# Performance work log

Measured on AMD Instinct MI355X. Metric: run time of the kernel, lower is better.

The kernel has to match this reference:

```python
import jax, jax.numpy as jnp
import numpy as np

B, T, C = 2, 2048, 1024
H, DK, DV = 16, 64, 64


def setup_inputs() -> dict:
    key = jax.random.key(0)
    ks = jax.random.split(key, 12)
    p = lambda k, shape: (jax.random.normal(k, shape, dtype=jnp.float32) * 0.02)
    Q = jax.random.normal(ks[0], (B, T, C), dtype=jnp.float32)
    K = jax.random.normal(ks[1], (B, T, C), dtype=jnp.float32)
    V = jax.random.normal(ks[2], (B, T, C), dtype=jnp.float32)
    Wq, bq = p(ks[3], (C, H * DK)), p(ks[4], (H * DK,))
    Wk, bk = p(ks[5], (C, H * DK)), p(ks[6], (H * DK,))
    Wv, bv = p(ks[7], (C, H * DV)), p(ks[8], (H * DV,))
    Wo, bo = p(ks[9], (H * DV, C)), p(ks[10], (C,))
    # additive causal mask, broadcastable to (B, H, T, T)
    causal = jnp.tril(jnp.ones((T, T), dtype=bool))
    mask = jnp.where(causal, 0.0, -1e9).astype(jnp.float32)[None, None]
    return {"Q": Q, "K": K, "V": V, "Wq": Wq, "bq": bq, "Wk": Wk, "bk": bk,
            "Wv": Wv, "bv": bv, "Wo": Wo, "bo": bo, "mask": mask}


def reference(Q, K, V, Wq, bq, Wk, bk, Wv, bv, Wo, bo, mask):
    def split(x, d):  # (B,T,H*d) -> (B,H,T,d)
        return x.reshape(B, T, H, d).transpose(0, 2, 1, 3)

    q = split(Q @ Wq + bq, DK)
    k = split(K @ Wk + bk, DK)
    v = split(V @ Wv + bv, DV)
    # NOTE: faithful to source — mask added BEFORE scaling by 1/sqrt(dk)
    scores = (jnp.einsum('bhqd,bhkd->bhqk', q, k) + mask) / float(np.sqrt(DK))
    attn = jax.nn.softmax(scores, axis=-1)
    out = jnp.einsum('bhqk,bhkd->bhqd', attn, v)  # (B,H,T,DV)
    out = out.transpose(0, 2, 1, 3).reshape(B, T, H * DV)
    return out @ Wo + bo
```

## Files before the change

### kernel.cpp

```cpp
#include <hip/hip_runtime.h>
#include <cstdint>
#include <cstddef>

#define TB 2
#define TT 2048
#define TC 1024
#define TH 16
#define TD 64
#define MROWS (TB*TT)

typedef __attribute__((ext_vector_type(8))) short bf16x8;
typedef __attribute__((ext_vector_type(4))) float f32x4;

#define QSCL2 0.18033688011112042f
#define MASKL2 (-1.8033688e8f)

__device__ __forceinline__ unsigned short f2bf(float f) {
  union { float f; unsigned int u; } x; x.f = f;
  unsigned int r = x.u + 0x7fffu + ((x.u >> 16) & 1u);
  return (unsigned short)(r >> 16);
}

__device__ __forceinline__ void gload16(const void* g, void* l) {
  __builtin_amdgcn_global_load_lds((const __attribute__((address_space(1))) void*)g,
                                   (__attribute__((address_space(3))) void*)l, 16, 0, 0);
}

#define WAITVM(N) do { asm volatile("s_waitcnt vmcnt(" #N ")" ::: "memory"); \
                       __builtin_amdgcn_sched_barrier(0); } while (0)

__device__ __forceinline__ float exp2h(float x) {
  float r;
  asm("v_exp_f32 %0, %1" : "=v"(r) : "v"(x));
  return r;
}

__global__ __launch_bounds__(256) void wtrans4_kernel(
    const float* __restrict__ W0, const float* __restrict__ W1,
    const float* __restrict__ W2, const float* __restrict__ W3,
    unsigned short* __restrict__ T0, unsigned short* __restrict__ T1,
    unsigned short* __restrict__ T2, unsigned short* __restrict__ T3) {
  const int z = blockIdx.z;
  const float* W = z == 0 ? W0 : (z == 1 ? W1 : (z == 2 ? W2 : W3));
  unsigned short* WT = z == 0 ? T0 : (z == 1 ? T1 : (z == 2 ? T2 : T3));
  __shared__ float ts[32][33];
  int tx = threadIdx.x & 31, ty = threadIdx.x >> 5;
  int n0 = blockIdx.x * 32, k0 = blockIdx.y * 32;
#pragma unroll
  for (int r = 0; r < 32; r += 8)
    ts[ty + r][tx] = W[(size_t)(k0 + ty + r) * TC + n0 + tx];
  __syncthreads();
#pragma unroll
  for (int r = 0; r < 32; r += 8)
    WT[(size_t)(n0 + ty + r) * TC + k0 + tx] = f2bf(ts[tx][ty + r]);
}

__global__ __launch_bounds__(256) void cast3_kernel(
    const float* __restrict__ A, const float* __restrict__ B, const float* __restrict__ C,
    unsigned short* __restrict__ oa, unsigned short* __restrict__ ob,
    unsigned short* __restrict__ oc) {
  const int z = blockIdx.y;
  const float* in = z == 0 ? A : (z == 1 ? B : C);
  unsigned short* out = z == 0 ? oa : (z == 1 ? ob : oc);
  int i = (blockIdx.x * 256 + threadIdx.x) * 8;
  float4 f0 = *(const float4*)(in + i);
  float4 f1 = *(const float4*)(in + i + 4);
  union { unsigned short u[8]; int4 v; } pk;
  pk.u[0] = f2bf(f0.x); pk.u[1] = f2bf(f0.y); pk.u[2] = f2bf(f0.z); pk.u[3] = f2bf(f0.w);
  pk.u[4] = f2bf(f1.x); pk.u[5] = f2bf(f1.y); pk.u[6] = f2bf(f1.z); pk.u[7] = f2bf(f1.w);
  *(int4*)(out + i) = pk.v;
}

__device__ __forceinline__ void gemm_core(const unsigned short* __restrict__ A,
                                          const unsigned short* __restrict__ Bt,
                                          int m0, int n0,
                                          unsigned short (*As)[64], unsigned short (*Bs)[64],
                                          f32x4 acc[4][4]) {
  const int tid = threadIdx.x, wave = tid >> 6, lane = tid & 63;
  const int lh = lane & 15, lq = lane >> 4;
  const int wr = wave >> 1, wc = wave & 1;
  const int srow = lane >> 3;
  const int sseg = (lane & 7) ^ srow;

  for (int k0 = 0; k0 < TC; k0 += 64) {
    __syncthreads();
#pragma unroll
    for (int c = 0; c < 4; ++c) {
      const int chunk = wave * 4 + c;
      const int row = chunk * 8 + srow;
      gload16(A + (size_t)(m0 + row) * TC + k0 + sseg * 8, &As[chunk * 8][0]);
      gload16(Bt + (size_t)(n0 + row) * TC + k0 + sseg * 8, &Bs[chunk * 8][0]);
    }
    __syncthreads();
#pragma unroll
    for (int kk = 0; kk < 2; ++kk) {
      const int seg = kk * 4 + lq;
      bf16x8 a[4], b[4];
#pragma unroll
      for (int i = 0; i < 4; ++i) {
        int row = wr * 64 + i * 16 + lh;
        a[i] = *(const bf16x8*)&As[row][(seg ^ (row & 7)) << 3];
      }
#pragma unroll
      for (int j = 0; j < 4; ++j) {
        int row = wc * 64 + j * 16 + lh;
        b[j] = *(const bf16x8*)&Bs[row][(seg ^ (row & 7)) << 3];
      }
#pragma unroll
      for (int i = 0; i < 4; ++i)
#pragma unroll
        for (int j = 0; j < 4; ++j)
          acc[i][j] = __builtin_amdgcn_mfma_f32_16x16x32_bf16(a[i], b[j], acc[i][j], 0, 0, 0);
    }
  }
}

__global__ __launch_bounds__(256, 3)
void qkv_gemm_kernel(const unsigned short* __restrict__ Aq, const unsigned short* __restrict__ Ak,
                     const unsigned short* __restrict__ Av,
                     const unsigned short* __restrict__ BTq, const unsigned short* __restrict__ BTk,
                     const unsigned short* __restrict__ BTv,
                     const float* __restrict__ bq, const float* __restrict__ bk,
                     const float* __restrict__ bv,
                     unsigned short* __restrict__ Oq, unsigned short* __restrict__ Ok,
                     unsigned short* __restrict__ Ov, int zbase) {
  __shared__ __attribute__((aligned(16))) unsigned short As[128][64];
  __shared__ __attribute__((aligned(16))) unsigned short Bs[128][64];
  const int z = blockIdx.z + zbase;
  const unsigned short* A  = z == 0 ? Aq  : (z == 1 ? Ak  : Av);
  const unsigned short* Bt = z == 0 ? BTq : (z == 1 ? BTk : BTv);
  const float* bias        = z == 0 ? bq  : (z == 1 ? bk  : bv);
  unsigned short* Out      = z == 0 ? Oq  : (z == 1 ? Ok  : Ov);

  const int tid = threadIdx.x, wave = tid >> 6, lane = tid & 63;
  const int lh = lane & 15, lq = lane >> 4;
  const int wr = wave >> 1, wc = wave & 1;
  const int m0 = blockIdx.y * 128, n0 = blockIdx.x * 128;
  const f32x4 vzero = {0.f, 0.f, 0.f, 0.f};
  f32x4 acc[4][4];
#pragma unroll
  for (int i = 0; i < 4; ++i)
#pragma unroll
    for (int j = 0; j < 4; ++j) acc[i][j] = vzero;

  gemm_core(A, Bt, m0, n0, As, Bs, acc);

#pragma unroll
  for (int i = 0; i < 4; ++i)
#pragma unroll
    for (int j = 0; j < 4; ++j) {
      const int cg = n0 + wc * 64 + j * 16 + lh;
      const float bb = bias[cg];
      if (z == 2) {
        int rg0 = m0 + wr * 64 + i * 16 + lq * 4;
        int bidx = rg0 >> 11, t0 = rg0 & (TT - 1);
        int h = cg >> 6, d = cg & 63;
        unsigned long long pk = 0ull;
#pragma unroll
        for (int r = 0; r < 4; ++r)
          pk |= (unsigned long long)f2bf(acc[i][j][r] + bb) << (16 * r);
        *(unsigned long long*)(Out + ((size_t)((bidx * TH + h) * TD + d)) * TT + t0) = pk;
      } else {
#pragma unroll
        for (int r = 0; r < 4; ++r) {
          int rg = m0 + wr * 64 + i * 16 + lq * 4 + r;
          int bidx = rg >> 11, t = rg & (TT - 1);
          int h = cg >> 6, d = cg & 63;
          Out[((size_t)((bidx * TH + h) * TT + t)) * TD + d] = f2bf(acc[i][j][r] + bb);
        }
      }
    }
}

__global__ __launch_bounds__(256, 2)
void oproj_gemm_kernel(const unsigned short* __restrict__ A, const unsigned short* __restrict__ Bt,
                       const float* __restrict__ bias, float* __restrict__ Out) {
  __shared__ __attribute__((aligned(16))) unsigned short As[128][64];
  __shared__ __attribute__((aligned(16))) unsigned short Bs[64][64];
  const int tid = threadIdx.x, wave = tid >> 6, lane = tid & 63;
  const int lh = lane & 15, lq = lane >> 4;
  const int wr = wave >> 1, wc = wave & 1;
  const int m0 = blockIdx.y * 128, n0 = blockIdx.x * 64;
  const int srow = lane >> 3, sseg = (lane & 7) ^ srow;
  const f32x4 vzero = {0.f, 0.f, 0.f, 0.f};
  f32x4 acc[4][2];
#pragma unroll
  for (int i = 0; i < 4; ++i)
#pragma unroll
    for (int j = 0; j < 2; ++j) acc[i][j] = vzero;

  for (int k0 = 0; k0 < TC; k0 += 64) {
    __syncthreads();
#pragma unroll
    for (int c = 0; c < 4; ++c) {
      const int chunk = wave * 4 + c;
      const int row = chunk * 8 + srow;
      gload16(A + (size_t)(m0 + row) * TC + k0 + sseg * 8, &As[chunk * 8][0]);
    }
#pragma unroll
    for (int c = 0; c < 2; ++c) {
      const int chunk = wave * 2 + c;
      const int row = chunk * 8 + srow;
      gload16(Bt + (size_t)(n0 + row) * TC + k0 + sseg * 8, &Bs[chunk * 8][0]);
    }
    __syncthreads();
#pragma unroll
    for (int kk = 0; kk < 2; ++kk) {
      const int seg = kk * 4 + lq;
      bf16x8 a[4], b[2];
#pragma unroll
      for (int i = 0; i < 4; ++i) {
        int row = wr * 64 + i * 16 + lh;
        a[i] = *(const bf16x8*)&As[row][(seg ^ (row & 7)) << 3];
      }
#pragma unroll
      for (int j = 0; j < 2; ++j) {
        int row = wc * 32 + j * 16 + lh;
        b[j] = *(const bf16x8*)&Bs[row][(seg ^ (row & 7)) << 3];
      }
#pragma unroll
      for (int i = 0; i < 4; ++i)
#pragma unroll
        for (int j = 0; j < 2; ++j)
          acc[i][j] = __builtin_amdgcn_mfma_f32_16x16x32_bf16(a[i], b[j], acc[i][j], 0, 0, 0);
    }
  }

#pragma unroll
  for (int i = 0; i < 4; ++i)
#pragma unroll
    for (int j = 0; j < 2; ++j) {
      const int cg = n0 + wc * 32 + j * 16 + lh;
      const float bb = bias[cg];
#pragma unroll
      for (int r = 0; r < 4; ++r) {
        int rg = m0 + wr * 64 + i * 16 + lq * 4 + r;
        Out[(size_t)rg * TC + cg] = acc[i][j][r] + bb;
      }
    }
}

__global__ __launch_bounds__(256, 2)
void attn_kernel(const unsigned short* __restrict__ qb, const unsigned short* __restrict__ kb,
                 const unsigned short* __restrict__ vtb, unsigned short* __restrict__ ob) {
  __shared__ __attribute__((aligned(16))) unsigned short Qs[64][64];
  __shared__ __attribute__((aligned(16))) unsigned short Ks[3][64][64];
  __shared__ __attribute__((aligned(16))) unsigned short Vs[3][64][64];
  const int tid = threadIdx.x, wave = tid >> 6, lane = tid & 63;
  const int lh = lane & 15, lq = lane >> 4;
  const int srow = lane >> 3, sseg = (lane & 7) ^ srow;
  const int swzA = lh & 7;

  const int lid = blockIdx.x;
  const int xcd = lid & 7, idx = lid >> 3;
  const int bh = xcd * 4 + (idx & 3);
  const int pair = idx >> 2;
  const size_t qkb = (size_t)bh * TT * TD;
  const size_t vob = (size_t)bh * TD * TT;
  const int bidx = bh >> 4, h = bh & 15;
  const f32x4 vzero = {0.f, 0.f, 0.f, 0.f};

  union { unsigned short u[8]; bf16x8 v; } onef;
#pragma unroll
  for (int i = 0; i < 8; ++i) onef.u[i] = 0x3F80;

  auto stageKV = [&](int buf, int t) {
    const int kv0 = t * 64;
#pragma unroll
    for (int c = 0; c < 2; ++c) {
      const int chunk = wave * 2 + c;
      const int row = chunk * 8 + srow;
      gload16(kb + qkb + (size_t)(kv0 + row) * TD + sseg * 8, &Ks[buf][chunk * 8][0]);
      gload16(vtb + vob + (size_t)row * TT + kv0 + sseg * 8, &Vs[buf][chunk * 8][0]);
    }
  };

#pragma unroll 1
  for (int sub = 0; sub < 2; ++sub) {
    const int bx = (sub == 0) ? (31 - pair) : pair;
    const int q0 = bx * 64;
    const int nt = bx + 1;
    const int q_g = q0 + wave * 16 + lh;

#pragma unroll
    for (int c = 0; c < 2; ++c) {
      const int chunk = wave * 2 + c;
      const int row = chunk * 8 + srow;
      gload16(qb + qkb + (size_t)(q0 + row) * TD + sseg * 8, &Qs[chunk * 8][0]);
    }
    stageKV(0, 0);
    if (nt > 1) { stageKV(1, 1); WAITVM(4); }
    else        { WAITVM(0); }
    __builtin_amdgcn_s_barrier();

    bf16x8 aq[2];
    {
      const int row = wave * 16 + lh;
#pragma unroll
      for (int kk = 0; kk < 2; ++kk)
        aq[kk] = *(const bf16x8*)&Qs[row][((kk * 4 + lq) ^ (row & 7)) << 3];
    }
    f32x4 oacc[4], lacc = vzero;
#pragma unroll
    for (int jt = 0; jt < 4; ++jt) oacc[jt] = vzero;

    for (int t = 0; t < nt; ++t) {
      const int cur = t % 3;
      const int kv0 = t * 64;
      if (t + 2 < nt)      { stageKV((t + 2) % 3, t + 2); WAITVM(8); }
      else if (t + 1 < nt) { WAITVM(4); }
      else                 { WAITVM(0); }
      __builtin_amdgcn_s_barrier();

      f32x4 accS[4];
#pragma unroll
      for (int j = 0; j < 4; ++j) accS[j] = vzero;
      __builtin_amdgcn_s_setprio(1);
#pragma unroll
      for (int kk = 0; kk < 2; ++kk) {
#pragma unroll
        for (int j = 0; j < 4; ++j) {
          bf16x8 bk = *(const bf16x8*)&Ks[cur][j * 16 + lh][((kk * 4 + lq) ^ swzA) << 3];
          accS[j] = __builtin_amdgcn_mfma_f32_16x16x32_bf16(bk, aq[kk], accS[j], 0, 0, 0);
        }
      }
      __builtin_amdgcn_s_setprio(0);

      float p_[16];
      if (t == bx) {
#pragma unroll
        for (int j = 0; j < 4; ++j)
#pragma unroll
          for (int r = 0; r < 4; ++r) {
            const int kvg = kv0 + j * 16 + lq * 4 + r;
            p_[j * 4 + r] = fmaf(accS[j][r], QSCL2, (kvg <= q_g) ? 0.f : MASKL2);
          }
      } else {
#pragma unroll
        for (int j = 0; j < 4; ++j)
#pragma unroll
          for (int r = 0; r < 4; ++r)
            p_[j * 4 + r] = accS[j][r] * QSCL2;
      }
#pragma unroll
      for (int i = 0; i < 16; ++i) p_[i] = exp2h(p_[i]);

      unsigned Dw[8];
#pragma unroll
      for (int j = 0; j < 4; ++j)
#pragma unroll
        for (int tt = 0; tt < 2; ++tt)
          asm("v_cvt_pk_bf16_f32 %0, %1, %2"
              : "=v"(Dw[j * 2 + tt]) : "v"(p_[j * 4 + 2 * tt]), "v"(p_[j * 4 + 2 * tt + 1]));
#pragma unroll
      for (int ks = 0; ks < 2; ++ks) {
        unsigned x0 = Dw[(2 * ks) * 2 + 0], y0 = Dw[(2 * ks + 1) * 2 + 0];
        unsigned x1 = Dw[(2 * ks) * 2 + 1], y1 = Dw[(2 * ks + 1) * 2 + 1];
        asm("v_permlane32_swap_b32 %0, %1" : "+v"(x0), "+v"(y0));
        asm("v_permlane16_swap_b32 %0, %1" : "+v"(x0), "+v"(y0));
        asm("v_permlane32_swap_b32 %0, %1" : "+v"(x1), "+v"(y1));
        asm("v_permlane16_swap_b32 %0, %1" : "+v"(x1), "+v"(y1));
        union { unsigned u[4]; bf16x8 v; } pb;
        pb.u[0] = x0; pb.u[1] = x1; pb.u[2] = y0; pb.u[3] = y1;
        __builtin_amdgcn_s_setprio(1);
#pragma unroll
        for (int jt = 0; jt < 4; ++jt) {
          bf16x8 av = *(const bf16x8*)&Vs[cur][jt * 16 + lh][((ks * 4 + lq) ^ swzA) << 3];
          oacc[jt] = __builtin_amdgcn_mfma_f32_16x16x32_bf16(av, pb.v, oacc[jt], 0, 0, 0);
        }
        lacc = __builtin_amdgcn_mfma_f32_16x16x32_bf16(onef.v, pb.v, lacc, 0, 0, 0);
        __builtin_amdgcn_s_setprio(0);
      }
      __builtin_amdgcn_s_barrier();
    }

    const float inv = 1.f / lacc[0];
    unsigned short* orow = ob + ((size_t)(bidx * TT + q_g)) * TC + h * TD;
#pragma unroll
    for (int jt = 0; jt < 4; ++jt) {
      unsigned long long pk = 0ull;
#pragma unroll
      for (int r = 0; r < 4; ++r)
        pk |= (unsigned long long)f2bf(oacc[jt][r] * inv) << (16 * r);
      *(unsigned long long*)(orow + jt * 16 + lq * 4) = pk;
    }
  }
}

extern "C" void kernel_launch(void* const* d_in, const int* in_sizes, int n_in,
                              void* d_out, int out_size, void* d_ws, size_t ws_size,
                              hipStream_t stream) {
  const float* Q  = (const float*)d_in[0];
  const float* K  = (const float*)d_in[1];
  const float* V  = (const float*)d_in[2];
  const float* Wq = (const float*)d_in[3];
  const float* bq = (const float*)d_in[4];
  const float* Wk = (const float*)d_in[5];
  const float* bk = (const float*)d_in[6];
  const float* Wv = (const float*)d_in[7];
  const float* bv = (const float*)d_in[8];
  const float* Wo = (const float*)d_in[9];
  const float* bo = (const float*)d_in[10];
  float* out = (float*)d_out;

  char* ws = (char*)d_ws;
  const size_t MB = 1ull << 20;
  unsigned short* WqT = (unsigned short*)(ws + 0 * MB);
  unsigned short* WkT = (unsigned short*)(ws + 2 * MB);
  unsigned short* WvT = (unsigned short*)(ws + 4 * MB);
  unsigned short* WoT = (unsigned short*)(ws + 6 * MB);

  const bool fat = ws_size >= 56 * MB;
  unsigned short *qc, *kc, *vc, *qbuf, *kbuf, *vtbuf, *aout;
  if (fat) {
    qc    = (unsigned short*)(ws + 8 * MB);
    kc    = (unsigned short*)(ws + 16 * MB);
    vc    = (unsigned short*)(ws + 24 * MB);
    qbuf  = (unsigned short*)(ws + 32 * MB);
    kbuf  = (unsigned short*)(ws + 40 * MB);
    vtbuf = (unsigned short*)(ws + 48 * MB);
    aout  = qc;
  } else {
    qc = kc = vc = (unsigned short*)(ws + 8 * MB);
    qbuf  = (unsigned short*)(ws + 16 * MB);
    kbuf  = (unsigned short*)(ws + 24 * MB);
    vtbuf = (unsigned short*)(ws + 32 * MB);
    aout  = qc;
  }

  dim3 blk(256);
  wtrans4_kernel<<<dim3(32, 32, 4), blk, 0, stream>>>(Wq, Wk, Wv, Wo, WqT, WkT, WvT, WoT);

  const int castGrid = MROWS * TC / (256 * 8);
  if (fat) {
    cast3_kernel<<<dim3(castGrid, 3), blk, 0, stream>>>(Q, K, V, qc, kc, vc);
    qkv_gemm_kernel<<<dim3(TC / 128, MROWS / 128, 3), blk, 0, stream>>>(
        qc, kc, vc, WqT, WkT, WvT, bq, bk, bv, qbuf, kbuf, vtbuf, 0);
  } else {
    cast3_kernel<<<dim3(castGrid, 1), blk, 0, stream>>>(Q, Q, Q, qc, qc, qc);
    qkv_gemm_kernel<<<dim3(TC / 128, MROWS / 128, 1), blk, 0, stream>>>(
        qc, qc, qc, WqT, WkT, WvT, bq, bk, bv, qbuf, kbuf, vtbuf, 0);
    cast3_kernel<<<dim3(castGrid, 1), blk, 0, stream>>>(K, K, K, kc, kc, kc);
    qkv_gemm_kernel<<<dim3(TC / 128, MROWS / 128, 1), blk, 0, stream>>>(
        kc, kc, kc, WqT, WkT, WvT, bq, bk, bv, qbuf, kbuf, vtbuf, 1);
    cast3_kernel<<<dim3(castGrid, 1), blk, 0, stream>>>(V, V, V, vc, vc, vc);
    qkv_gemm_kernel<<<dim3(TC / 128, MROWS / 128, 1), blk, 0, stream>>>(
        vc, vc, vc, WqT, WkT, WvT, bq, bk, bv, qbuf, kbuf, vtbuf, 2);
  }

  attn_kernel<<<dim3(512), blk, 0, stream>>>(qbuf, kbuf, vtbuf, aout);

  oproj_gemm_kernel<<<dim3(TC / 64, MROWS / 128), blk, 0, stream>>>(aout, WoT, bo, out);
}
```

Baseline: 111.1 us.

## Fuse prep kernels, swizzle GEMM tiles per XCD, split attention into one tile per block

Merges the weight-transpose and input-cast kernels into a single prep launch to cut launch overhead. Remaps the GEMM block indices so blocks sharing A/B tiles land on the same XCD for L2 reuse. Restructures attention from two paired query tiles per block (512 blocks) to one tile per block (1024 blocks), dropping K/V staging from triple to double buffering and raising occupancy to 4 blocks per CU. This trades pipelining depth and the paired-tile load balance for more parallelism and lower LDS use.

```diff
diff --git a/kernel.cpp b/kernel.cpp
--- a/kernel.cpp
+++ b/kernel.cpp
@@ -33,6 +33,46 @@
   float r;
   asm("v_exp_f32 %0, %1" : "=v"(r) : "v"(x));
   return r;
+}
+
+__global__ __launch_bounds__(256) void prep_kernel(
+    const float* __restrict__ W0, const float* __restrict__ W1,
+    const float* __restrict__ W2, const float* __restrict__ W3,
+    unsigned short* __restrict__ T0, unsigned short* __restrict__ T1,
+    unsigned short* __restrict__ T2, unsigned short* __restrict__ T3,
+    const float* __restrict__ Q, const float* __restrict__ K, const float* __restrict__ V,
+    unsigned short* __restrict__ qc, unsigned short* __restrict__ kc,
+    unsigned short* __restrict__ vc) {
+  const int z = blockIdx.z;
+  if (z < 4) {
+    const float* W = z == 0 ? W0 : (z == 1 ? W1 : (z == 2 ? W2 : W3));
+    unsigned short* WT = z == 0 ? T0 : (z == 1 ? T1 : (z == 2 ? T2 : T3));
+    __shared__ float ts[32][33];
+    int tx = threadIdx.x & 31, ty = threadIdx.x >> 5;
+    int n0 = blockIdx.x * 32, k0 = blockIdx.y * 32;
+#pragma unroll
+    for (int r = 0; r < 32; r += 8)
+      ts[ty + r][tx] = W[(size_t)(k0 + ty + r) * TC + n0 + tx];
+    __syncthreads();
+#pragma unroll
+    for (int r = 0; r < 32; r += 8)
+      WT[(size_t)(n0 + ty + r) * TC + k0 + tx] = f2bf(ts[tx][ty + r]);
+  } else {
+    const int zt = z - 4;
+    const float* in = zt == 0 ? Q : (zt == 1 ? K : V);
+    unsigned short* out = zt == 0 ? qc : (zt == 1 ? kc : vc);
+    const int lb = blockIdx.y * 32 + blockIdx.x;
+#pragma unroll
+    for (int c = 0; c < 2; ++c) {
+      int i = lb * 4096 + c * 2048 + threadIdx.x * 8;
+      float4 f0 = *(const float4*)(in + i);
+      float4 f1 = *(const float4*)(in + i + 4);
+      union { unsigned short u[8]; int4 v; } pk;
+      pk.u[0] = f2bf(f0.x); pk.u[1] = f2bf(f0.y); pk.u[2] = f2bf(f0.z); pk.u[3] = f2bf(f0.w);
+      pk.u[4] = f2bf(f1.x); pk.u[5] = f2bf(f1.y); pk.u[6] = f2bf(f1.z); pk.u[7] = f2bf(f1.w);
+      *(int4*)(out + i) = pk.v;
+    }
+  }
 }
 
 __global__ __launch_bounds__(256) void wtrans4_kernel(
@@ -132,10 +172,13 @@
   const float* bias        = z == 0 ? bq  : (z == 1 ? bk  : bv);
   unsigned short* Out      = z == 0 ? Oq  : (z == 1 ? Ok  : Ov);
 
+  const int lin = blockIdx.y * 8 + blockIdx.x;
+  const int swz = (lin & 7) * 32 + (lin >> 3);
+  const int m0 = (swz >> 3) * 128, n0 = (swz & 7) * 128;
+
   const int tid = threadIdx.x, wave = tid >> 6, lane = tid & 63;
   const int lh = lane & 15, lq = lane >> 4;
   const int wr = wave >> 1, wc = wave & 1;
-  const int m0 = blockIdx.y * 128, n0 = blockIdx.x * 128;
   const f32x4 vzero = {0.f, 0.f, 0.f, 0.f};
   f32x4 acc[4][4];
 #pragma unroll
@@ -177,10 +220,13 @@
                        const float* __restrict__ bias, float* __restrict__ Out) {
   __shared__ __attribute__((aligned(16))) unsigned short As[128][64];
   __shared__ __attribute__((aligned(16))) unsigned short Bs[64][64];
+  const int lin = blockIdx.y * 16 + blockIdx.x;
+  const int swz = (lin & 7) * 64 + (lin >> 3);
+  const int m0 = (swz >> 4) * 128, n0 = (swz & 15) * 64;
+
   const int tid = threadIdx.x, wave = tid >> 6, lane = tid & 63;
   const int lh = lane & 15, lq = lane >> 4;
   const int wr = wave >> 1, wc = wave & 1;
-  const int m0 = blockIdx.y * 128, n0 = blockIdx.x * 64;
   const int srow = lane >> 3, sseg = (lane & 7) ^ srow;
   const f32x4 vzero = {0.f, 0.f, 0.f, 0.f};
   f32x4 acc[4][2];
@@ -240,21 +286,20 @@
     }
 }
 
-__global__ __launch_bounds__(256, 2)
+__global__ __launch_bounds__(256, 4)
 void attn_kernel(const unsigned short* __restrict__ qb, const unsigned short* __restrict__ kb,
                  const unsigned short* __restrict__ vtb, unsigned short* __restrict__ ob) {
   __shared__ __attribute__((aligned(16))) unsigned short Qs[64][64];
-  __shared__ __attribute__((aligned(16))) unsigned short Ks[3][64][64];
-  __shared__ __attribute__((aligned(16))) unsigned short Vs[3][64][64];
+  __shared__ __attribute__((aligned(16))) unsigned short Ks[2][64][64];
+  __shared__ __attribute__((aligned(16))) unsigned short Vs[2][64][64];
   const int tid = threadIdx.x, wave = tid >> 6, lane = tid & 63;
   const int lh = lane & 15, lq = lane >> 4;
   const int srow = lane >> 3, sseg = (lane & 7) ^ srow;
   const int swzA = lh & 7;
 
-  const int lid = blockIdx.x;
-  const int xcd = lid & 7, idx = lid >> 3;
-  const int bh = xcd * 4 + (idx & 3);
-  const int pair = idx >> 2;
+  const int id = blockIdx.x;
+  const int bh = (id & 7) * 4 + ((id >> 3) & 3);
+  const int bx = 31 - (id >> 5);
   const size_t qkb = (size_t)bh * TT * TD;
   const size_t vob = (size_t)bh * TD * TT;
   const int bidx = bh >> 4, h = bh & 15;
@@ -275,115 +320,108 @@
     }
   };
 
-#pragma unroll 1
-  for (int sub = 0; sub < 2; ++sub) {
-    const int bx = (sub == 0) ? (31 - pair) : pair;
-    const int q0 = bx * 64;
-    const int nt = bx + 1;
-    const int q_g = q0 + wave * 16 + lh;
-
-#pragma unroll
-    for (int c = 0; c < 2; ++c) {
-      const int chunk = wave * 2 + c;
-      const int row = chunk * 8 + srow;
-      gload16(qb + qkb + (size_t)(q0 + row) * TD + sseg * 8, &Qs[chunk * 8][0]);
-    }
-    stageKV(0, 0);
-    if (nt > 1) { stageKV(1, 1); WAITVM(4); }
-    else        { WAITVM(0); }
+  const int q0 = bx * 64;
+  const int nt = bx + 1;
+  const int q_g = q0 + wave * 16 + lh;
+
+#pragma unroll
+  for (int c = 0; c < 2; ++c) {
+    const int chunk = wave * 2 + c;
+    const int row = chunk * 8 + srow;
+    gload16(qb + qkb + (size_t)(q0 + row) * TD + sseg * 8, &Qs[chunk * 8][0]);
+  }
+  stageKV(0, 0);
+  if (nt > 1) { stageKV(1, 1); WAITVM(4); }
+  else        { WAITVM(0); }
+  bf16x8 aq[2];
+  {
+    const int row = wave * 16 + lh;
+#pragma unroll
+    for (int kk = 0; kk < 2; ++kk)
+      aq[kk] = *(const bf16x8*)&Qs[row][((kk * 4 + lq) ^ (row & 7)) << 3];
+  }
+  f32x4 oacc[4], lacc = vzero;
+#pragma unroll
+  for (int jt = 0; jt < 4; ++jt) oacc[jt] = vzero;
+
+  for (int t = 0; t < nt; ++t) {
+    const int cur = t & 1;
+    const int kv0 = t * 64;
+    if (t >= 1 && t + 1 < nt) stageKV(cur ^ 1, t + 1);
+    if (t + 1 < nt) { WAITVM(4); } else { WAITVM(0); }
     __builtin_amdgcn_s_barrier();
 
-    bf16x8 aq[2];
-    {
-      const int row = wave * 16 + lh;
-#pragma unroll
-      for (int kk = 0; kk < 2; ++kk)
-        aq[kk] = *(const bf16x8*)&Qs[row][((kk * 4 + lq) ^ (row & 7)) << 3];
-    }
-    f32x4 oacc[4], lacc = vzero;
-#pragma unroll
-    for (int jt = 0; jt < 4; ++jt) oacc[jt] = vzero;
-
-    for (int t = 0; t < nt; ++t) {
-      const int cur = t % 3;
-      const int kv0 = t * 64;
-      if (t + 2 < nt)      { stageKV((t + 2) % 3, t + 2); WAITVM(8); }
-      else if (t + 1 < nt) { WAITVM(4); }
-      else                 { WAITVM(0); }
-      __builtin_amdgcn_s_barrier();
-
-      f32x4 accS[4];
-#pragma unroll
-      for (int j = 0; j < 4; ++j) accS[j] = vzero;
+    f32x4 accS[4];
+#pragma unroll
+    for (int j = 0; j < 4; ++j) accS[j] = vzero;
+    __builtin_amdgcn_s_setprio(1);
+#pragma unroll
+    for (int kk = 0; kk < 2; ++kk) {
+#pragma unroll
+      for (int j = 0; j < 4; ++j) {
+        bf16x8 bk = *(const bf16x8*)&Ks[cur][j * 16 + lh][((kk * 4 + lq) ^ swzA) << 3];
+        accS[j] = __builtin_amdgcn_mfma_f32_16x16x32_bf16(bk, aq[kk], accS[j], 0, 0, 0);
+      }
+    }
+    __builtin_amdgcn_s_setprio(0);
+
+    float p_[16];
+    if (t == bx) {
+#pragma unroll
+      for (int j = 0; j < 4; ++j)
+#pragma unroll
+        for (int r = 0; r < 4; ++r) {
+          const int kvg = kv0 + j * 16 + lq * 4 + r;
+          p_[j * 4 + r] = fmaf(accS[j][r], QSCL2, (kvg <= q_g) ? 0.f : MASKL2);
+        }
+    } else {
+#pragma unroll
+      for (int j = 0; j < 4; ++j)
+#pragma unroll
+        for (int r = 0; r < 4; ++r)
+          p_[j * 4 + r] = accS[j][r] * QSCL2;
+    }
+#pragma unroll
+    for (int i = 0; i < 16; ++i) p_[i] = exp2h(p_[i]);
+
+    unsigned Dw[8];
+#pragma unroll
+    for (int j = 0; j < 4; ++j)
+#pragma unroll
+      for (int tt = 0; tt < 2; ++tt)
+        asm("v_cvt_pk_bf16_f32 %0, %1, %2"
+            : "=v"(Dw[j * 2 + tt]) : "v"(p_[j * 4 + 2 * tt]), "v"(p_[j * 4 + 2 * tt + 1]));
+#pragma unroll
+    for (int ks = 0; ks < 2; ++ks) {
+      unsigned x0 = Dw[(2 * ks) * 2 + 0], y0 = Dw[(2 * ks + 1) * 2 + 0];
+      unsigned x1 = Dw[(2 * ks) * 2 + 1], y1 = Dw[(2 * ks + 1) * 2 + 1];
+      asm("v_permlane32_swap_b32 %0, %1" : "+v"(x0), "+v"(y0));
+      asm("v_permlane16_swap_b32 %0, %1" : "+v"(x0), "+v"(y0));
+      asm("v_permlane32_swap_b32 %0, %1" : "+v"(x1), "+v"(y1));
+      asm("v_permlane16_swap_b32 %0, %1" : "+v"(x1), "+v"(y1));
+      union { unsigned u[4]; bf16x8 v; } pb;
+      pb.u[0] = x0; pb.u[1] = x1; pb.u[2] = y0; pb.u[3] = y1;
       __builtin_amdgcn_s_setprio(1);
 #pragma unroll
-      for (int kk = 0; kk < 2; ++kk) {
-#pragma unroll
-        for (int j = 0; j < 4; ++j) {
-          bf16x8 bk = *(const bf16x8*)&Ks[cur][j * 16 + lh][((kk * 4 + lq) ^ swzA) << 3];
-          accS[j] = __builtin_amdgcn_mfma_f32_16x16x32_bf16(bk, aq[kk], accS[j], 0, 0, 0);
-        }
-      }
+      for (int jt = 0; jt < 4; ++jt) {
+        bf16x8 av = *(const bf16x8*)&Vs[cur][jt * 16 + lh][((ks * 4 + lq) ^ swzA) << 3];
+        oacc[jt] = __builtin_amdgcn_mfma_f32_16x16x32_bf16(av, pb.v, oacc[jt], 0, 0, 0);
+      }
+      lacc = __builtin_amdgcn_mfma_f32_16x16x32_bf16(onef.v, pb.v, lacc, 0, 0, 0);
       __builtin_amdgcn_s_setprio(0);
-
-      float p_[16];
-      if (t == bx) {
-#pragma unroll
-        for (int j = 0; j < 4; ++j)
-#pragma unroll
-          for (int r = 0; r < 4; ++r) {
-            const int kvg = kv0 + j * 16 + lq * 4 + r;
-            p_[j * 4 + r] = fmaf(accS[j][r], QSCL2, (kvg <= q_g) ? 0.f : MASKL2);
-          }
-      } else {
-#pragma unroll
-        for (int j = 0; j < 4; ++j)
-#pragma unroll
-          for (int r = 0; r < 4; ++r)
-            p_[j * 4 + r] = accS[j][r] * QSCL2;
-      }
-#pragma unroll
-      for (int i = 0; i < 16; ++i) p_[i] = exp2h(p_[i]);
-
-      unsigned Dw[8];
-#pragma unroll
-      for (int j = 0; j < 4; ++j)
-#pragma unroll
-        for (int tt = 0; tt < 2; ++tt)
-          asm("v_cvt_pk_bf16_f32 %0, %1, %2"
-              : "=v"(Dw[j * 2 + tt]) : "v"(p_[j * 4 + 2 * tt]), "v"(p_[j * 4 + 2 * tt + 1]));
-#pragma unroll
-      for (int ks = 0; ks < 2; ++ks) {
-        unsigned x0 = Dw[(2 * ks) * 2 + 0], y0 = Dw[(2 * ks + 1) * 2 + 0];
-        unsigned x1 = Dw[(2 * ks) * 2 + 1], y1 = Dw[(2 * ks + 1) * 2 + 1];
-        asm("v_permlane32_swap_b32 %0, %1" : "+v"(x0), "+v"(y0));
-        asm("v_permlane16_swap_b32 %0, %1" : "+v"(x0), "+v"(y0));
-        asm("v_permlane32_swap_b32 %0, %1" : "+v"(x1), "+v"(y1));
-        asm("v_permlane16_swap_b32 %0, %1" : "+v"(x1), "+v"(y1));
-        union { unsigned u[4]; bf16x8 v; } pb;
-        pb.u[0] = x0; pb.u[1] = x1; pb.u[2] = y0; pb.u[3] = y1;
-        __builtin_amdgcn_s_setprio(1);
-#pragma unroll
-        for (int jt = 0; jt < 4; ++jt) {
-          bf16x8 av = *(const bf16x8*)&Vs[cur][jt * 16 + lh][((ks * 4 + lq) ^ swzA) << 3];
-          oacc[jt] = __builtin_amdgcn_mfma_f32_16x16x32_bf16(av, pb.v, oacc[jt], 0, 0, 0);
-        }
-        lacc = __builtin_amdgcn_mfma_f32_16x16x32_bf16(onef.v, pb.v, lacc, 0, 0, 0);
-        __builtin_amdgcn_s_setprio(0);
-      }
-      __builtin_amdgcn_s_barrier();
-    }
-
-    const float inv = 1.f / lacc[0];
-    unsigned short* orow = ob + ((size_t)(bidx * TT + q_g)) * TC + h * TD;
-#pragma unroll
-    for (int jt = 0; jt < 4; ++jt) {
-      unsigned long long pk = 0ull;
-#pragma unroll
-      for (int r = 0; r < 4; ++r)
-        pk |= (unsigned long long)f2bf(oacc[jt][r] * inv) << (16 * r);
-      *(unsigned long long*)(orow + jt * 16 + lq * 4) = pk;
-    }
+    }
+    __builtin_amdgcn_s_barrier();
+  }
+
+  const float inv = 1.f / lacc[0];
+  unsigned short* orow = ob + ((size_t)(bidx * TT + q_g)) * TC + h * TD;
+#pragma unroll
+  for (int jt = 0; jt < 4; ++jt) {
+    unsigned long long pk = 0ull;
+#pragma unroll
+    for (int r = 0; r < 4; ++r)
+      pk |= (unsigned long long)f2bf(oacc[jt][r] * inv) << (16 * r);
+    *(unsigned long long*)(orow + jt * 16 + lq * 4) = pk;
   }
 }
 
@@ -429,26 +467,26 @@
   }
 
   dim3 blk(256);
-  wtrans4_kernel<<<dim3(32, 32, 4), blk, 0, stream>>>(Wq, Wk, Wv, Wo, WqT, WkT, WvT, WoT);
-
-  const int castGrid = MROWS * TC / (256 * 8);
   if (fat) {
-    cast3_kernel<<<dim3(castGrid, 3), blk, 0, stream>>>(Q, K, V, qc, kc, vc);
-    qkv_gemm_kernel<<<dim3(TC / 128, MROWS / 128, 3), blk, 0, stream>>>(
+    prep_kernel<<<dim3(32, 32, 7), blk, 0, stream>>>(
+        Wq, Wk, Wv, Wo, WqT, WkT, WvT, WoT, Q, K, V, qc, kc, vc);
+    qkv_gemm_kernel<<<dim3(8, 32, 3), blk, 0, stream>>>(
         qc, kc, vc, WqT, WkT, WvT, bq, bk, bv, qbuf, kbuf, vtbuf, 0);
   } else {
+    const int castGrid = MROWS * TC / (256 * 8);
+    wtrans4_kernel<<<dim3(32, 32, 4), blk, 0, stream>>>(Wq, Wk, Wv, Wo, WqT, WkT, WvT, WoT);
     cast3_kernel<<<dim3(castGrid, 1), blk, 0, stream>>>(Q, Q, Q, qc, qc, qc);
-    qkv_gemm_kernel<<<dim3(TC / 128, MROWS / 128, 1), blk, 0, stream>>>(
+    qkv_gemm_kernel<<<dim3(8, 32, 1), blk, 0, stream>>>(
         qc, qc, qc, WqT, WkT, WvT, bq, bk, bv, qbuf, kbuf, vtbuf, 0);
     cast3_kernel<<<dim3(castGrid, 1), blk, 0, stream>>>(K, K, K, kc, kc, kc);
-    qkv_gemm_kernel<<<dim3(TC / 128, MROWS / 128, 1), blk, 0, stream>>>(
+    qkv_gemm_kernel<<<dim3(8, 32, 1), blk, 0, stream>>>(
         kc, kc, kc, WqT, WkT, WvT, bq, bk, bv, qbuf, kbuf, vtbuf, 1);
     cast3_kernel<<<dim3(castGrid, 1), blk, 0, stream>>>(V, V, V, vc, vc, vc);
-    qkv_gemm_kernel<<<dim3(TC / 128, MROWS / 128, 1), blk, 0, stream>>>(
+    qkv_gemm_kernel<<<dim3(8, 32, 1), blk, 0, stream>>>(
         vc, vc, vc, WqT, WkT, WvT, bq, bk, bv, qbuf, kbuf, vtbuf, 2);
   }
 
-  attn_kernel<<<dim3(512), blk, 0, stream>>>(qbuf, kbuf, vtbuf, aout);
-
-  oproj_gemm_kernel<<<dim3(TC / 64, MROWS / 128), blk, 0, stream>>>(aout, WoT, bo, out);
-}
+  attn_kernel<<<dim3(1024), blk, 0, stream>>>(qbuf, kbuf, vtbuf, aout);
+
+  oproj_gemm_kernel<<<dim3(16, 32), blk, 0, stream>>>(aout, WoT, bo, out);
+}
```

New measurement: 106.2 us. 4.4% less time.
